# Optimization experiments

Measured on AMD Instinct MI355X. Metric: run time of the kernel, lower is better.

Reference implementation:

```python
import jax, jax.numpy as jnp
import numpy as np

N, E, IN_DIM, HID, OUT, H = 50000, 800000, 128, 96, 96, 4
C1, C2 = HID // H, OUT // H
EPS = 1e-5

def _lin(key, out_f, in_f):
    kw, kb = jax.random.split(key)
    s = 1.0 / np.sqrt(in_f)
    W = jax.random.uniform(kw, (out_f, in_f), jnp.float32, -s, s)
    b = jax.random.uniform(kb, (out_f,), jnp.float32, -s, s)
    return W, b

def setup_inputs() -> dict:
    key = jax.random.key(0)
    ks = jax.random.split(key, 16)
    x = jax.random.normal(ks[0], (N, IN_DIM), jnp.float32)
    edge_index = jax.random.randint(ks[1], (2, E), 0, N, jnp.int64)
    Wq1, bq1 = _lin(ks[2], HID, IN_DIM)
    Wk1, bk1 = _lin(ks[3], HID, IN_DIM)
    Wv1, bv1 = _lin(ks[4], HID, IN_DIM)
    Ws1, bs1 = _lin(ks[5], HID, IN_DIM)
    Wb1 = _lin(ks[6], 1, 3 * HID)[0]
    Wq2, bq2 = _lin(ks[7], OUT, HID)
    Wk2, bk2 = _lin(ks[8], OUT, HID)
    Wv2, bv2 = _lin(ks[9], OUT, HID)
    Ws2, bs2 = _lin(ks[10], OUT, HID)
    Wb2 = _lin(ks[11], 1, 3 * OUT)[0]
    gamma = jnp.ones((OUT,), jnp.float32)
    beta = jnp.zeros((OUT,), jnp.float32)
    return dict(x=x, edge_index=edge_index, Wq1=Wq1, bq1=bq1, Wk1=Wk1, bk1=bk1,
                Wv1=Wv1, bv1=bv1, Ws1=Ws1, bs1=bs1, Wb1=Wb1,
                Wq2=Wq2, bq2=bq2, Wk2=Wk2, bk2=bk2, Wv2=Wv2, bv2=bv2,
                Ws2=Ws2, bs2=bs2, Wb2=Wb2, gamma=gamma, beta=beta)

def transformer_conv(x, src, dst, Wq, bq, Wk, bk, Wv, bv, Ws, bs, Wb, heads, ch):
    n = x.shape[0]
    q = (x @ Wq.T + bq).reshape(n, heads, ch)
    k = (x @ Wk.T + bk).reshape(n, heads, ch)
    v = (x @ Wv.T + bv).reshape(n, heads, ch)
    # per-edge attention logits [E, H]
    alpha = jnp.einsum('ehc,ehc->eh', q[dst], k[src]) / jnp.sqrt(jnp.float32(ch))
    amax = jax.ops.segment_max(alpha, dst, num_segments=n)
    a = jnp.exp(alpha - amax[dst])
    denom = jax.ops.segment_sum(a, dst, num_segments=n)
    a = a / denom[dst]
    msg = v[src] * a[:, :, None]                       # [E, H, C]
    out = jax.ops.segment_sum(msg, dst, num_segments=n).reshape(n, heads * ch)
    x_r = x @ Ws.T + bs                                # root/skip transform
    g = jax.nn.sigmoid(jnp.concatenate([out, x_r, out - x_r], -1) @ Wb.T)
    return g * x_r + (1.0 - g) * out

def reference(x, edge_index, Wq1, bq1, Wk1, bk1, Wv1, bv1, Ws1, bs1, Wb1,
              Wq2, bq2, Wk2, bk2, Wv2, bv2, Ws2, bs2, Wb2, gamma, beta):
    src, dst = edge_index[0], edge_index[1]
    h = transformer_conv(x, src, dst, Wq1, bq1, Wk1, bk1, Wv1, bv1, Ws1, bs1, Wb1, H, C1)
    h = jax.nn.gelu(h, approximate=False)
    h = transformer_conv(h, src, dst, Wq2, bq2, Wk2, bk2, Wv2, bv2, Ws2, bs2, Wb2, H, C2)
    mu = jnp.mean(h, axis=-1, keepdims=True)
    var = jnp.mean(jnp.square(h - mu), axis=-1, keepdims=True)
    return (h - mu) / jnp.sqrt(var + EPS) * gamma + beta
```

## Files before the change

kernel.cpp:

```cpp
#include <hip/hip_runtime.h>
#include <hip/hip_bf16.h>
#include <hip/hip_fp16.h>
#include <math.h>

constexpr int NN = 50000;
constexpr int EE = 800000;
constexpr int SCAN_NB = (NN + 255) / 256;
constexpr int HISTB   = (EE + 255) / 256;
constexpr int FILLB   = (EE + 255) / 256;
constexpr int GEMMB   = ((NN + 15) / 16 + 3) / 4;

typedef short v8s __attribute__((ext_vector_type(8)));
typedef float v4f __attribute__((ext_vector_type(4)));

__device__ __forceinline__ short f2b(float f){
  __hip_bfloat16 h = __float2bfloat16(f);
  return *reinterpret_cast<short*>(&h);
}
__device__ __forceinline__ __half2 u2h2(unsigned int u){
  union { unsigned int u; __half2 h; } c; c.u = u; return c.h;
}

__global__ __launch_bounds__(256) void histpack_kernel(
    const int* __restrict__ ei, int* __restrict__ deg,
    const float* __restrict__ Wq1, const float* __restrict__ bq1,
    const float* __restrict__ Wk1, const float* __restrict__ bk1,
    const float* __restrict__ Wv1, const float* __restrict__ bv1,
    const float* __restrict__ Ws1, const float* __restrict__ bs1,
    const float* __restrict__ Wq2, const float* __restrict__ bq2,
    const float* __restrict__ Wk2, const float* __restrict__ bk2,
    const float* __restrict__ Wv2, const float* __restrict__ bv2,
    const float* __restrict__ Ws2, const float* __restrict__ bs2,
    const float* __restrict__ Wb1, const float* __restrict__ Wb2,
    short* __restrict__ Wcat1, float* __restrict__ bcat1,
    short* __restrict__ Wcat2, float* __restrict__ bcat2,
    float* __restrict__ wa1, float* __restrict__ wc1,
    float* __restrict__ wa2, float* __restrict__ wc2){
  int b = blockIdx.x;
  if (b < HISTB){
    int e = b * 256 + threadIdx.x;
    if (e < EE) atomicAdd(&deg[ei[EE + e] << 4], 1);
  } else if (b < HISTB + 768){
    int c = b - HISTB;
    int layer = c / 384, cc = c % 384;
    int which = cc / 96, r = cc % 96;
    const float *Wsel, *bsel;
    int K; short* Wd; float* bd;
    if (layer == 0){
      Wsel = which == 0 ? Wq1 : which == 1 ? Wk1 : which == 2 ? Wv1 : Ws1;
      bsel = which == 0 ? bq1 : which == 1 ? bk1 : which == 2 ? bv1 : bs1;
      K = 128; Wd = Wcat1; bd = bcat1;
    } else {
      Wsel = which == 0 ? Wq2 : which == 1 ? Wk2 : which == 2 ? Wv2 : Ws2;
      bsel = which == 0 ? bq2 : which == 1 ? bk2 : which == 2 ? bv2 : bs2;
      K = 96; Wd = Wcat2; bd = bcat2;
    }
    for (int k = threadIdx.x; k < K; k += blockDim.x)
      Wd[(size_t)cc * K + k] = f2b(Wsel[(size_t)r * K + k]);
    if (threadIdx.x == 0) bd[cc] = bsel[r];
  } else {
    int t = threadIdx.x;
    if (t < 96){
      wa1[t] = Wb1[t] + Wb1[192 + t];
      wc1[t] = Wb1[96 + t] - Wb1[192 + t];
    } else if (t < 192){
      int f = t - 96;
      wa2[f] = Wb2[f] + Wb2[192 + f];
      wc2[f] = Wb2[96 + f] - Wb2[192 + f];
    }
  }
}

__global__ __launch_bounds__(256) void partial_sum_kernel(const int* __restrict__ deg,
                                                          int* __restrict__ psum){
  int b = blockIdx.x, tid = threadIdx.x, lane = tid & 63, wv = tid >> 6;
  int i = b * 256 + tid;
  int v = (i < NN) ? deg[i << 4] : 0;
  #pragma unroll
  for (int m = 1; m < 64; m <<= 1) v += __shfl_xor(v, m);
  __shared__ int ws[4];
  if (lane == 0) ws[wv] = v;
  __syncthreads();
  if (tid == 0) psum[b] = ws[0] + ws[1] + ws[2] + ws[3];
}

__global__ __launch_bounds__(256) void scan_partials_kernel(int* __restrict__ psum){
  int tid = threadIdx.x, lane = tid & 63, wv = tid >> 6;
  int own = (tid < SCAN_NB) ? psum[tid] : 0;
  int v = own;
  #pragma unroll
  for (int off = 1; off < 64; off <<= 1){
    int t = __shfl_up(v, off);
    if (lane >= off) v += t;
  }
  __shared__ int ws[4];
  if (lane == 63) ws[wv] = v;
  __syncthreads();
  int add = 0;
  #pragma unroll
  for (int w = 0; w < 4; w++) if (w < wv) add += ws[w];
  if (tid < SCAN_NB) psum[tid] = v + add - own;
}

__global__ __launch_bounds__(256) void final_scan_kernel(const int* __restrict__ deg,
                                                         const int* __restrict__ psum,
                                                         int* __restrict__ row_ptr,
                                                         int* __restrict__ cursor){
  int b = blockIdx.x, tid = threadIdx.x, lane = tid & 63, wv = tid >> 6;
  int i = b * 256 + tid;
  int d = (i < NN) ? deg[i << 4] : 0;
  int v = d;
  #pragma unroll
  for (int off = 1; off < 64; off <<= 1){
    int t = __shfl_up(v, off);
    if (lane >= off) v += t;
  }
  __shared__ int ws[4];
  if (lane == 63) ws[wv] = v;
  __syncthreads();
  int add = psum[b];
  #pragma unroll
  for (int w = 0; w < 4; w++) if (w < wv) add += ws[w];
  if (i < NN){
    row_ptr[i + 1] = add + v;
    cursor[i << 4] = add + v - d;
  }
  if (i == 0) row_ptr[0] = 0;
}

template<int K, bool AF32>
__device__ __forceinline__ void gemm_body(int tile, const void* __restrict__ Ain,
                                          const short* __restrict__ Wcat,
                                          const float* __restrict__ bcat,
                                          __half* __restrict__ qsh,
                                          __half* __restrict__ kvb, int M){
  constexpr int NK = K / 32;
  if (tile * 16 >= M) return;
  const int lane = threadIdx.x & 63;
  const int rt = tile * 16;
  const int fr = lane & 15, fk = lane >> 4;
  const int arow = rt + fr;

  v8s a[NK];
  if constexpr (AF32){
    const float* A = (const float*)Ain;
    #pragma unroll
    for (int ks = 0; ks < NK; ks++){
      const float* p = A + (size_t)arow * K + ks * 32 + fk * 8;
      float4 a0 = *(const float4*)p;
      float4 a1 = *(const float4*)(p + 4);
      v8s o;
      o[0] = f2b(a0.x); o[1] = f2b(a0.y); o[2] = f2b(a0.z); o[3] = f2b(a0.w);
      o[4] = f2b(a1.x); o[5] = f2b(a1.y); o[6] = f2b(a1.z); o[7] = f2b(a1.w);
      a[ks] = o;
    }
  } else {
    const short* A = (const short*)Ain;
    #pragma unroll
    for (int ks = 0; ks < NK; ks++)
      a[ks] = *(const v8s*)(A + (size_t)arow * K + ks * 32 + fk * 8);
  }

  #pragma unroll 4
  for (int p = 0; p < 24; p++){
    const int c0 = p * 16;
    const int gcol = c0 + fr;
    v4f acc = (v4f){0.f, 0.f, 0.f, 0.f};
    #pragma unroll
    for (int ks = 0; ks < NK; ks++){
      v8s b = *(const v8s*)(Wcat + (size_t)gcol * K + ks * 32 + fk * 8);
      acc = __builtin_amdgcn_mfma_f32_16x16x32_bf16(a[ks], b, acc, 0, 0, 0);
    }
    const float bias = bcat[gcol];
    if (c0 < 96){
      #pragma unroll
      for (int r = 0; r < 4; r++)
        qsh[(size_t)(rt + fk * 4 + r) * 192 + gcol] = __float2half(acc[r] + bias);
    } else if (c0 < 192){
      #pragma unroll
      for (int r = 0; r < 4; r++)
        kvb[(size_t)(rt + fk * 4 + r) * 192 + (gcol - 96)] = __float2half(acc[r] + bias);
    } else if (c0 < 288){
      #pragma unroll
      for (int r = 0; r < 4; r++)
        kvb[(size_t)(rt + fk * 4 + r) * 192 + 96 + (gcol - 192)] = __float2half(acc[r] + bias);
    } else {
      #pragma unroll
      for (int r = 0; r < 4; r++)
        qsh[(size_t)(rt + fk * 4 + r) * 192 + 96 + (gcol - 288)] = __float2half(acc[r] + bias);
    }
  }
}

template<int K, bool AF32>
__global__ __launch_bounds__(256) void fillgemm_kernel(
    const int* __restrict__ ei, int* __restrict__ cursor,
    unsigned short* __restrict__ col_src,
    const void* __restrict__ Ain, const short* __restrict__ Wcat,
    const float* __restrict__ bcat, __half* __restrict__ qsh,
    __half* __restrict__ kvb, int M){
  int b = blockIdx.x;
  if (b < FILLB){
    int e = b * 256 + threadIdx.x;
    if (e < EE){
      int src = ei[e], dst = ei[EE + e];
      int pos = atomicAdd(&cursor[dst << 4], 1);
      col_src[pos] = (unsigned short)src;
    }
  } else {
    int tile = (b - FILLB) * 4 + (threadIdx.x >> 6);
    gemm_body<K, AF32>(tile, Ain, Wcat, bcat, qsh, kvb, M);
  }
}

template<int K, bool AF32>
__global__ __launch_bounds__(256) void gemm_kernel(const void* __restrict__ Ain,
                                                   const short* __restrict__ Wcat,
                                                   const float* __restrict__ bcat,
                                                   __half* __restrict__ qsh,
                                                   __half* __restrict__ kvb, int M){
  int tile = blockIdx.x * 4 + (threadIdx.x >> 6);
  gemm_body<K, AF32>(tile, Ain, Wcat, bcat, qsh, kvb, M);
}

__global__ __launch_bounds__(256) void attn_kernel(
    const __half* __restrict__ qs, const __half* __restrict__ kv,
    const int* __restrict__ row_ptr, const unsigned short* __restrict__ col_src,
    const float* __restrict__ wa, const float* __restrict__ wc,
    const float* __restrict__ gamma, const float* __restrict__ beta,
    float* __restrict__ outp, short* __restrict__ h1b, int mode){
  const int lane = threadIdx.x & 63;
  const int wid  = threadIdx.x >> 6;
  const int n = blockIdx.x * 4 + wid;
  if (n >= NN) return;
  const int h_a = lane & 3;
  const int g_a = lane >> 2;
  const int l_v = lane & 15;
  const int vg  = lane >> 4;
  const int h_v = l_v >> 2;
  const char* kvc = (const char*)kv;
  const char* qsc = (const char*)qs;

  __half2 qh[12];
  {
    const uint4* qp = (const uint4*)(qsc + (size_t)n * 384 + h_a * 48);
    uint4 a0 = qp[0], a1 = qp[1], a2 = qp[2];
    qh[0] = u2h2(a0.x); qh[1] = u2h2(a0.y); qh[2]  = u2h2(a0.z); qh[3]  = u2h2(a0.w);
    qh[4] = u2h2(a1.x); qh[5] = u2h2(a1.y); qh[6]  = u2h2(a1.z); qh[7]  = u2h2(a1.w);
    qh[8] = u2h2(a2.x); qh[9] = u2h2(a2.y); qh[10] = u2h2(a2.z); qh[11] = u2h2(a2.w);
  }
  const int rs = row_ptr[n], re = row_ptr[n + 1];
  float m = -INFINITY, s = 0.f;
  float acc[6] = {0.f, 0.f, 0.f, 0.f, 0.f, 0.f};

  for (int cb = rs; cb < re; cb += 16){
    const int cn = re - cb;
    int srcv = col_src[cb + min(g_a, cn - 1)];
    int sb[4];
    #pragma unroll
    for (int st = 0; st < 4; st++)
      sb[st] = __shfl(srcv, 4 * min(st * 4 + vg, cn - 1));
    unsigned int vd[4][3];
    #pragma unroll
    for (int st = 0; st < 4; st++){
      const unsigned int* vp =
        (const unsigned int*)(kvc + (size_t)sb[st] * 384 + 192 + 12 * l_v);
      vd[st][0] = vp[0]; vd[st][1] = vp[1]; vd[st][2] = vp[2];
    }
    const uint4* kp = (const uint4*)(kvc + (size_t)srcv * 384 + h_a * 48);
    uint4 u0 = kp[0], u1 = kp[1], u2 = kp[2];
    __half2 d0 = __floats2half2_rn(0.f, 0.f), d1 = d0;
    d0 = __hfma2(qh[0],  u2h2(u0.x), d0); d1 = __hfma2(qh[1],  u2h2(u0.y), d1);
    d0 = __hfma2(qh[2],  u2h2(u0.z), d0); d1 = __hfma2(qh[3],  u2h2(u0.w), d1);
    d0 = __hfma2(qh[4],  u2h2(u1.x), d0); d1 = __hfma2(qh[5],  u2h2(u1.y), d1);
    d0 = __hfma2(qh[6],  u2h2(u1.z), d0); d1 = __hfma2(qh[7],  u2h2(u1.w), d1);
    d0 = __hfma2(qh[8],  u2h2(u2.x), d0); d1 = __hfma2(qh[9],  u2h2(u2.y), d1);
    d0 = __hfma2(qh[10], u2h2(u2.z), d0); d1 = __hfma2(qh[11], u2h2(u2.w), d1);
    float dot = __low2float(d0) + __high2float(d0) + __low2float(d1) + __high2float(d1);
    float al = (g_a < cn) ? dot * 0.2041241452319315f : -INFINITY;

    float cm = al;
    cm = fmaxf(cm, __shfl_xor(cm, 4));
    cm = fmaxf(cm, __shfl_xor(cm, 8));
    cm = fmaxf(cm, __shfl_xor(cm, 16));
    cm = fmaxf(cm, __shfl_xor(cm, 32));
    float nm = fmaxf(m, cm);
    float r  = __expf(m - nm);
    float e  = __expf(al - nm);
    float cs = e;
    cs += __shfl_xor(cs, 4);
    cs += __shfl_xor(cs, 8);
    cs += __shfl_xor(cs, 16);
    cs += __shfl_xor(cs, 32);
    s = s * r + cs;
    m = nm;

    float rv = __shfl(r, h_v);
    __half2 ch0 = __floats2half2_rn(0.f, 0.f), ch1 = ch0, ch2 = ch0;
    #pragma unroll
    for (int st = 0; st < 4; st++){
      int eidx = st * 4 + vg;
      float w = __shfl(e, 4 * min(eidx, cn - 1) + h_v);
      if (eidx >= cn) w = 0.f;
      __half2 w2 = __float2half2_rn(w);
      ch0 = __hfma2(w2, u2h2(vd[st][0]), ch0);
      ch1 = __hfma2(w2, u2h2(vd[st][1]), ch1);
      ch2 = __hfma2(w2, u2h2(vd[st][2]), ch2);
    }
    acc[0] = fmaf(acc[0], rv, __low2float(ch0));
    acc[1] = fmaf(acc[1], rv, __high2float(ch0));
    acc[2] = fmaf(acc[2], rv, __low2float(ch1));
    acc[3] = fmaf(acc[3], rv, __high2float(ch1));
    acc[4] = fmaf(acc[4], rv, __low2float(ch2));
    acc[5] = fmaf(acc[5], rv, __high2float(ch2));
  }

  #pragma unroll
  for (int i = 0; i < 6; i++){
    acc[i] += __shfl_xor(acc[i], 16);
    acc[i] += __shfl_xor(acc[i], 32);
  }
  float sv  = __shfl(s, h_v);
  float inv = (re > rs) ? 1.0f / sv : 0.f;
  float o[6], xr[6];
  #pragma unroll
  for (int i = 0; i < 6; i++) o[i] = acc[i] * inv;
  {
    const unsigned int* xp = (const unsigned int*)(qsc + (size_t)n * 384 + 192 + 12 * l_v);
    unsigned int x0 = xp[0], x1 = xp[1], x2 = xp[2];
    xr[0] = __low2float(u2h2(x0)); xr[1] = __high2float(u2h2(x0));
    xr[2] = __low2float(u2h2(x1)); xr[3] = __high2float(u2h2(x1));
    xr[4] = __low2float(u2h2(x2)); xr[5] = __high2float(u2h2(x2));
  }

  float p = 0.f;
  #pragma unroll
  for (int i = 0; i < 6; i++){
    int f = 6 * l_v + i;
    p = fmaf(o[i], wa[f], p);
    p = fmaf(xr[i], wc[f], p);
  }
  p += __shfl_xor(p, 1);
  p += __shfl_xor(p, 2);
  p += __shfl_xor(p, 4);
  p += __shfl_xor(p, 8);
  float g = 1.0f / (1.0f + __expf(-p));
  float y[6];
  #pragma unroll
  for (int i = 0; i < 6; i++) y[i] = fmaf(g, xr[i] - o[i], o[i]);

  if (mode == 0){
    #pragma unroll
    for (int i = 0; i < 6; i++)
      y[i] = 0.5f * y[i] * (1.0f + erff(y[i] * 0.7071067811865475f));
    if (vg == 0){
      short* op = h1b + (size_t)n * 96 + 6 * l_v;
      #pragma unroll
      for (int i = 0; i < 6; i++) op[i] = f2b(y[i]);
    }
  } else {
    float ssum = y[0] + y[1] + y[2] + y[3] + y[4] + y[5];
    ssum += __shfl_xor(ssum, 1);
    ssum += __shfl_xor(ssum, 2);
    ssum += __shfl_xor(ssum, 4);
    ssum += __shfl_xor(ssum, 8);
    float mu = ssum * (1.0f / 96.0f);
    float vsum = 0.f;
    #pragma unroll
    for (int i = 0; i < 6; i++){ float d = y[i] - mu; vsum += d * d; }
    vsum += __shfl_xor(vsum, 1);
    vsum += __shfl_xor(vsum, 2);
    vsum += __shfl_xor(vsum, 4);
    vsum += __shfl_xor(vsum, 8);
    float invs = rsqrtf(vsum * (1.0f / 96.0f) + 1e-5f);
    if (vg == 0){
      float* op = outp + (size_t)n * 96 + 6 * l_v;
      #pragma unroll
      for (int i = 0; i < 6; i++){
        int f = 6 * l_v + i;
        op[i] = (y[i] - mu) * invs * gamma[f] + beta[f];
      }
    }
  }
}

extern "C" void kernel_launch(void* const* d_in, const int* in_sizes, int n_in,
                              void* d_out, int out_size, void* d_ws, size_t ws_size,
                              hipStream_t stream){
  const float* x    = (const float*)d_in[0];
  const int*   ei   = (const int*)d_in[1];
  const float* Wq1  = (const float*)d_in[2];
  const float* bq1  = (const float*)d_in[3];
  const float* Wk1  = (const float*)d_in[4];
  const float* bk1  = (const float*)d_in[5];
  const float* Wv1  = (const float*)d_in[6];
  const float* bv1  = (const float*)d_in[7];
  const float* Ws1  = (const float*)d_in[8];
  const float* bs1  = (const float*)d_in[9];
  const float* Wb1  = (const float*)d_in[10];
  const float* Wq2  = (const float*)d_in[11];
  const float* bq2  = (const float*)d_in[12];
  const float* Wk2  = (const float*)d_in[13];
  const float* bk2  = (const float*)d_in[14];
  const float* Wv2  = (const float*)d_in[15];
  const float* bv2  = (const float*)d_in[16];
  const float* Ws2  = (const float*)d_in[17];
  const float* bs2  = (const float*)d_in[18];
  const float* Wb2  = (const float*)d_in[19];
  const float* gamma = (const float*)d_in[20];
  const float* beta  = (const float*)d_in[21];
  float* out = (float*)d_out;

  char* ws = (char*)d_ws;
  size_t off = 0;
  auto take = [&](size_t b) -> void* {
    void* p = ws + off;
    off += (b + 255) & ~(size_t)255;
    return p;
  };
  __half* qs           = (__half*)take((size_t)NN * 192 * 2);
  __half* kvb          = (__half*)take((size_t)NN * 192 * 2);
  short* h1b           = (short*)take((size_t)NN * 96 * 2);
  short* Wcat1         = (short*)take((size_t)384 * 128 * 2);
  short* Wcat2         = (short*)take((size_t)384 * 96 * 2);
  float* bcat1         = (float*)take(384 * 4);
  float* bcat2         = (float*)take(384 * 4);
  float* wa1           = (float*)take(96 * 4);
  float* wc1           = (float*)take(96 * 4);
  float* wa2           = (float*)take(96 * 4);
  float* wc2           = (float*)take(96 * 4);
  int* deg             = (int*)take((size_t)NN * 64);
  int* cursor          = (int*)take((size_t)NN * 64);
  int* row_ptr         = (int*)take((size_t)(NN + 1) * 4);
  unsigned short* col_src = (unsigned short*)take((size_t)EE * 2);
  int* psum            = (int*)take((size_t)SCAN_NB * 4);

  hipMemsetAsync(deg, 0, (size_t)NN * 64, stream);
  histpack_kernel<<<HISTB + 768 + 1, 256, 0, stream>>>(
      ei, deg,
      Wq1, bq1, Wk1, bk1, Wv1, bv1, Ws1, bs1,
      Wq2, bq2, Wk2, bk2, Wv2, bv2, Ws2, bs2,
      Wb1, Wb2, Wcat1, bcat1, Wcat2, bcat2, wa1, wc1, wa2, wc2);
  partial_sum_kernel<<<SCAN_NB, 256, 0, stream>>>(deg, psum);
  scan_partials_kernel<<<1, 256, 0, stream>>>(psum);
  final_scan_kernel<<<SCAN_NB, 256, 0, stream>>>(deg, psum, row_ptr, cursor);

  fillgemm_kernel<128, true><<<FILLB + GEMMB, 256, 0, stream>>>(
      ei, cursor, col_src, x, Wcat1, bcat1, qs, kvb, NN);
  attn_kernel<<<(NN + 3) / 4, 256, 0, stream>>>(qs, kvb, row_ptr, col_src,
                                                wa1, wc1, nullptr, nullptr,
                                                nullptr, h1b, 0);
  gemm_kernel<96, false><<<GEMMB, 256, 0, stream>>>(h1b, Wcat2, bcat2, qs, kvb, NN);
  attn_kernel<<<(NN + 3) / 4, 256, 0, stream>>>(qs, kvb, row_ptr, col_src,
                                                wa2, wc2, gamma, beta,
                                                out, nullptr, 1);
}
```

Measured before the change: 285.0 us.

## Record edge slots during histogram to build CSR fill without a second atomic pass

```diff
diff --git a/kernel.cpp b/kernel.cpp
--- a/kernel.cpp
+++ b/kernel.cpp
@@ -7,7 +7,6 @@
 constexpr int EE = 800000;
 constexpr int SCAN_NB = (NN + 255) / 256;
 constexpr int HISTB   = (EE + 255) / 256;
-constexpr int FILLB   = (EE + 255) / 256;
 constexpr int GEMMB   = ((NN + 15) / 16 + 3) / 4;
 
 typedef short v8s __attribute__((ext_vector_type(8)));
@@ -22,7 +21,7 @@
 }
 
 __global__ __launch_bounds__(256) void histpack_kernel(
-    const int* __restrict__ ei, int* __restrict__ deg,
+    const int* __restrict__ ei, int* __restrict__ degC, int* __restrict__ epos,
     const float* __restrict__ Wq1, const float* __restrict__ bq1,
     const float* __restrict__ Wk1, const float* __restrict__ bk1,
     const float* __restrict__ Wv1, const float* __restrict__ bv1,
@@ -39,7 +38,12 @@
   int b = blockIdx.x;
   if (b < HISTB){
     int e = b * 256 + threadIdx.x;
-    if (e < EE) atomicAdd(&deg[ei[EE + e] << 4], 1);
+    if (e < EE){
+      int dst = ei[EE + e];
+      int c = b & 7;
+      int old = atomicAdd(&degC[c * NN + dst], 1);
+      epos[e] = (c << 28) | old;
+    }
   } else if (b < HISTB + 768){
     int c = b - HISTB;
     int layer = c / 384, cc = c % 384;
@@ -71,11 +75,15 @@
   }
 }
 
-__global__ __launch_bounds__(256) void partial_sum_kernel(const int* __restrict__ deg,
+__global__ __launch_bounds__(256) void partial_sum_kernel(const int* __restrict__ degC,
                                                           int* __restrict__ psum){
   int b = blockIdx.x, tid = threadIdx.x, lane = tid & 63, wv = tid >> 6;
   int i = b * 256 + tid;
-  int v = (i < NN) ? deg[i << 4] : 0;
+  int v = 0;
+  if (i < NN){
+    #pragma unroll
+    for (int c = 0; c < 8; c++) v += degC[c * NN + i];
+  }
   #pragma unroll
   for (int m = 1; m < 64; m <<= 1) v += __shfl_xor(v, m);
   __shared__ int ws[4];
@@ -102,13 +110,21 @@
   if (tid < SCAN_NB) psum[tid] = v + add - own;
 }
 
-__global__ __launch_bounds__(256) void final_scan_kernel(const int* __restrict__ deg,
+__global__ __launch_bounds__(256) void final_scan_kernel(const int* __restrict__ degC,
                                                          const int* __restrict__ psum,
                                                          int* __restrict__ row_ptr,
-                                                         int* __restrict__ cursor){
+                                                         int* __restrict__ base8){
   int b = blockIdx.x, tid = threadIdx.x, lane = tid & 63, wv = tid >> 6;
   int i = b * 256 + tid;
-  int d = (i < NN) ? deg[i << 4] : 0;
+  int dc[8];
+  int d = 0;
+  if (i < NN){
+    #pragma unroll
+    for (int c = 0; c < 8; c++){ dc[c] = degC[c * NN + i]; d += dc[c]; }
+  } else {
+    #pragma unroll
+    for (int c = 0; c < 8; c++) dc[c] = 0;
+  }
   int v = d;
   #pragma unroll
   for (int off = 1; off < 64; off <<= 1){
@@ -122,10 +138,29 @@
   #pragma unroll
   for (int w = 0; w < 4; w++) if (w < wv) add += ws[w];
   if (i < NN){
+    int start = add + v - d;
     row_ptr[i + 1] = add + v;
-    cursor[i << 4] = add + v - d;
+    int run = start;
+    #pragma unroll
+    for (int c = 0; c < 8; c++){
+      base8[(size_t)i * 8 + c] = run;
+      run += dc[c];
+    }
   }
   if (i == 0) row_ptr[0] = 0;
+}
+
+__global__ void fill_kernel(const int* __restrict__ ei, const int* __restrict__ epos,
+                            const int* __restrict__ base8,
+                            unsigned short* __restrict__ col_src){
+  int e = blockIdx.x * blockDim.x + threadIdx.x;
+  if (e < EE){
+    int src = ei[e], dst = ei[EE + e];
+    unsigned int u = (unsigned int)epos[e];
+    int c = u >> 28, cnt = u & 0x0FFFFFFF;
+    int pos = base8[(size_t)dst * 8 + c] + cnt;
+    col_src[pos] = (unsigned short)src;
+  }
 }
 
 template<int K, bool AF32>
@@ -189,27 +224,6 @@
       for (int r = 0; r < 4; r++)
         qsh[(size_t)(rt + fk * 4 + r) * 192 + 96 + (gcol - 288)] = __float2half(acc[r] + bias);
     }
-  }
-}
-
-template<int K, bool AF32>
-__global__ __launch_bounds__(256) void fillgemm_kernel(
-    const int* __restrict__ ei, int* __restrict__ cursor,
-    unsigned short* __restrict__ col_src,
-    const void* __restrict__ Ain, const short* __restrict__ Wcat,
-    const float* __restrict__ bcat, __half* __restrict__ qsh,
-    __half* __restrict__ kvb, int M){
-  int b = blockIdx.x;
-  if (b < FILLB){
-    int e = b * 256 + threadIdx.x;
-    if (e < EE){
-      int src = ei[e], dst = ei[EE + e];
-      int pos = atomicAdd(&cursor[dst << 4], 1);
-      col_src[pos] = (unsigned short)src;
-    }
-  } else {
-    int tile = (b - FILLB) * 4 + (threadIdx.x >> 6);
-    gemm_body<K, AF32>(tile, Ain, Wcat, bcat, qsh, kvb, M);
   }
 }
 
@@ -429,24 +443,25 @@
   float* wc1           = (float*)take(96 * 4);
   float* wa2           = (float*)take(96 * 4);
   float* wc2           = (float*)take(96 * 4);
-  int* deg             = (int*)take((size_t)NN * 64);
-  int* cursor          = (int*)take((size_t)NN * 64);
+  int* degC            = (int*)take((size_t)8 * NN * 4);
+  int* epos            = (int*)take((size_t)EE * 4);
+  int* base8           = (int*)take((size_t)NN * 8 * 4);
   int* row_ptr         = (int*)take((size_t)(NN + 1) * 4);
   unsigned short* col_src = (unsigned short*)take((size_t)EE * 2);
   int* psum            = (int*)take((size_t)SCAN_NB * 4);
 
-  hipMemsetAsync(deg, 0, (size_t)NN * 64, stream);
+  hipMemsetAsync(degC, 0, (size_t)8 * NN * 4, stream);
   histpack_kernel<<<HISTB + 768 + 1, 256, 0, stream>>>(
-      ei, deg,
+      ei, degC, epos,
       Wq1, bq1, Wk1, bk1, Wv1, bv1, Ws1, bs1,
       Wq2, bq2, Wk2, bk2, Wv2, bv2, Ws2, bs2,
       Wb1, Wb2, Wcat1, bcat1, Wcat2, bcat2, wa1, wc1, wa2, wc2);
-  partial_sum_kernel<<<SCAN_NB, 256, 0, stream>>>(deg, psum);
+  partial_sum_kernel<<<SCAN_NB, 256, 0, stream>>>(degC, psum);
   scan_partials_kernel<<<1, 256, 0, stream>>>(psum);
-  final_scan_kernel<<<SCAN_NB, 256, 0, stream>>>(deg, psum, row_ptr, cursor);
-
-  fillgemm_kernel<128, true><<<FILLB + GEMMB, 256, 0, stream>>>(
-      ei, cursor, col_src, x, Wcat1, bcat1, qs, kvb, NN);
+  final_scan_kernel<<<SCAN_NB, 256, 0, stream>>>(degC, psum, row_ptr, base8);
+  fill_kernel<<<(EE + 255) / 256, 256, 0, stream>>>(ei, epos, base8, col_src);
+
+  gemm_kernel<128, true><<<GEMMB, 256, 0, stream>>>(x, Wcat1, bcat1, qs, kvb, NN);
   attn_kernel<<<(NN + 3) / 4, 256, 0, stream>>>(qs, kvb, row_ptr, col_src,
                                                 wa1, wc1, nullptr, nullptr,
                                                 nullptr, h1b, 0);
```

New measurement: 244.5 us. 1.17x faster.
